# Optimization experiments

Measured on AMD Instinct MI355X. Metric: run time of the kernel, lower is better.

## Reference

```python
import jax, jax.numpy as jnp
import numpy as np

N = 768                       # atoms
E = N * (N - 1)               # complete directed graph edges
DIM = 64                      # hidden dim
CUT = 5.0                     # rbf high
NC = 50                       # n_centers = ceil(5/0.1)
ODIM = 1                      # output_dim
NCONV = 3
_centers_np = np.linspace(0.0, CUT, NC)
CENTERS = jnp.asarray(_centers_np, jnp.float32)
GAP = float(_centers_np[1] - _centers_np[0])
RO_IN = 2 * ODIM + NC         # readout input: 2*output_dim + rbf fan_out = 52


def softplus_bt(x, beta, thr):
    # torch.nn.Softplus(beta, threshold): linear above threshold
    bx = beta * x
    return jnp.where(bx > thr, x, jax.nn.softplus(bx) / beta)


def rbf(d):
    # exp(-(1/gap) * (d - mu_k)^2); d: (..., 1) -> (..., NC)
    return jnp.exp((-1.0 / GAP) * (d - CENTERS) ** 2)


def setup_inputs() -> dict:
    key = jax.random.key(0)
    ks = jax.random.split(key, 24)
    atom_types = jax.random.randint(ks[0], (N,), 0, 100)
    edge_distances = jax.random.uniform(ks[1], (E, 1), jnp.float32) * CUT
    # complete directed graph, edge order matches the nested i,j loop (i!=j)
    ii = np.repeat(np.arange(N), N)
    jj = np.tile(np.arange(N), N)
    m = ii != jj
    src = jnp.asarray(ii[m], jnp.int32)
    dst = jnp.asarray(jj[m], jnp.int32)

    def p(k, shape, fan):
        return jax.random.normal(k, shape, jnp.float32) / np.sqrt(fan)

    embedding = p(ks[2], (100, DIM), DIM).at[0].set(0.0)  # padding_idx=0
    L = NCONV
    return {
        'atom_types': atom_types, 'edge_distances': edge_distances,
        'src': src, 'dst': dst, 'embedding': embedding,
        'w1': p(ks[3], (L, DIM, DIM), DIM),                 # node_layer1 (no bias)
        'pw1': p(ks[4], (L, NC, DIM), NC), 'pb1': p(ks[5], (L, DIM), NC),
        'pw2': p(ks[6], (L, DIM, DIM), DIM), 'pb2': p(ks[7], (L, DIM), DIM),
        'qw1': p(ks[8], (L, DIM, DIM), DIM), 'qb1': p(ks[9], (L, DIM), DIM),
        'qw2': p(ks[10], (L, DIM, DIM), DIM), 'qb2': p(ks[11], (L, DIM), DIM),
        'au_w1': p(ks[12], (DIM, 64), DIM), 'au_b1': p(ks[13], (64,), DIM),
        'au_w2': p(ks[14], (64, ODIM), 64), 'au_b2': p(ks[15], (ODIM,), 64),
        'ro_w1': p(ks[16], (RO_IN, 64), RO_IN), 'ro_b1': p(ks[17], (64,), RO_IN),
        'ro_w2': p(ks[18], (64, 2), 64), 'ro_b2': p(ks[19], (2,), 64),
    }


def reference(atom_types, edge_distances, src, dst, embedding,
              w1, pw1, pb1, pw2, pb2, qw1, qb1, qw2, qb2,
              au_w1, au_b1, au_w2, au_b2, ro_w1, ro_b1, ro_w2, ro_b2):
    h = embedding[atom_types]                       # (N, DIM)
    rbf_out = rbf(edge_distances)                   # (E, NC)
    for l in range(NCONV):
        nw = h @ w1[l]                              # node weights (N, DIM)
        e = softplus_bt(rbf_out @ pw1[l] + pb1[l], 0.5, 14) @ pw2[l] + pb2[l]  # (E, DIM)
        msg = nw[src] * e                           # gather-mul (E, DIM)
        agg = jax.ops.segment_sum(msg, dst, num_segments=N)  # scatter-sum (N, DIM)
        upd = softplus_bt(agg @ qw1[l] + qb1[l], 0.5, 14) @ qw2[l] + qb2[l]
        h = h + upd
    # atom_update with ShiftSoftplus (beta=1, shift=2, threshold=20)
    ha = softplus_bt(h @ au_w1 + au_b1, 1.0, 20) - jnp.log(jnp.float32(2.0))
    ha = ha @ au_w2 + au_b2                         # (N, ODIM)
    # readout over all ordered pairs i!=j, in edge order == (src, dst)
    edge_feat = jnp.concatenate([ha[src], ha[dst], rbf_out], axis=-1)  # (E, 52)
    logits = jax.nn.relu(edge_feat @ ro_w1 + ro_b1) @ ro_w2 + ro_b2    # (E, 2)
    return jax.nn.softmax(logits, axis=-1)
```

## Files before the change

kernel.cpp:

```cpp
#include <hip/hip_runtime.h>
#include <hip/hip_fp16.h>

#define NATOMS 768
#define NM1    767
#define NEDGE  (768*767)
#define DIM    64
#define NC     50
#define GAPF   (5.0f/49.0f)
#define NIGAP  (-49.0f/5.0f)
#define G      512
#define STEPF  (5.0f/511.0f)
#define INVSTEP (511.0f/5.0f)
#define LN2F   0.693147180559945f

#define WS_H     0
#define WS_NWA   49152
#define WS_NWB   73728
#define WS_HA    98304
#define WS_DISTT 99328
#define WS_TT    689152

__device__ __forceinline__ float softplus05(float x) {
    float bx = 0.5f * x;
    return (bx > 14.0f) ? x : 2.0f * __logf(1.0f + __expf(bx));
}
__device__ __forceinline__ int lane_bcast_i(int v, int l) {
    return __builtin_amdgcn_readlane(v, l);
}
__device__ __forceinline__ float lane_bcast_f(float v, int l) {
    return __uint_as_float((unsigned)__builtin_amdgcn_readlane((int)__float_as_uint(v), l));
}

__global__ __launch_bounds__(256)
void k_pre(const int* __restrict__ types, const float* __restrict__ dist,
           const float* __restrict__ emb, const float* __restrict__ w1all,
           const float* __restrict__ pw1, const float* __restrict__ pb1,
           const float* __restrict__ pw2, const float* __restrict__ pb2,
           const float* __restrict__ row1, const float* __restrict__ rob1,
           float* __restrict__ ws) {
    __shared__ float s_t[4 * 64];
    const int tid = threadIdx.x, widx = tid >> 6, c = tid & 63;
    float*  h     = ws + WS_H;
    __half* nwh   = (__half*)(ws + WS_NWA);
    float*  distT = ws + WS_DISTT;
    __half* TTh   = (__half*)(ws + WS_TT);
    const int b = blockIdx.x;

    if (b < 512) {
        const int w = b * 4 + widx, tbl = w >> 9, g = w & 511;
        const float d = g * STEPF;
        float val;
        if (tbl < 3) {
            const float* W1 = pw1 + tbl * NC * DIM;
            float t1 = pb1[tbl * DIM + c];
            for (int k = 0; k < NC; ++k) {
                float x = d - GAPF * (float)k;
                t1 = fmaf(__expf(NIGAP * x * x), W1[k * DIM + c], t1);
            }
            s_t[widx * 64 + c] = softplus05(t1);
            const float* W2 = pw2 + tbl * DIM * DIM;
            val = pb2[tbl * DIM + c];
            #pragma unroll 8
            for (int k = 0; k < DIM; ++k)
                val = fmaf(s_t[widx * 64 + k], W2[k * DIM + c], val);
        } else {
            val = rob1[c];
            for (int k = 0; k < NC; ++k) {
                float x = d - GAPF * (float)k;
                val = fmaf(__expf(NIGAP * x * x), row1[(2 + k) * DIM + c], val);
            }
        }
        __half* TTt = TTh + tbl * (G * DIM * 2);
        TTt[(g * DIM + c) * 2] = __float2half(val);
        if (g > 0) TTt[((g - 1) * DIM + c) * 2 + 1] = __float2half(val);
    } else if (b < 704) {
        const int i = (b - 512) * 4 + widx;
        float hv = emb[types[i] * DIM + c];
        h[i * DIM + c] = hv;
        s_t[widx * 64 + c] = hv;
        float acc = 0.0f;
        #pragma unroll 8
        for (int k = 0; k < DIM; ++k)
            acc = fmaf(s_t[widx * 64 + k], w1all[k * DIM + c], acc);
        nwh[i * DIM + c] = __float2half(acc);
    } else {
        const int idx = (b - 704) * 256 + tid;
        const int j = idx / NATOMS, i = idx - j * NATOMS;
        distT[idx] = (i == j) ? 0.0f : dist[i * NM1 + (j - (j > i))];
    }
}

__global__ __launch_bounds__(512)
void k_edgeupd(const __half2* __restrict__ TTl, const float* __restrict__ distT,
               const __half* __restrict__ nwin,
               const float* __restrict__ qw1, const float* __restrict__ qb1,
               const float* __restrict__ qw2, const float* __restrict__ qb2,
               float* __restrict__ h,
               const float* __restrict__ wnext, __half* __restrict__ nwout,
               const float* __restrict__ auw1, const float* __restrict__ aub1,
               const float* __restrict__ auw2, const float* __restrict__ aub2,
               float* __restrict__ ha, int last) {
    __shared__ float s_part[8][64];
    __shared__ float s_upd[192];
    const int tid = threadIdx.x, widx = tid >> 6, c = tid & 63;
    const int j = blockIdx.x;
    const int s0 = widx * 96;

    const char* TTb = (const char*)TTl + c * 4;
    float csum = 0.0f;
    {
        float d = distT[j * NATOMS + s0 + c];
        float pos = d * INVSTEP;
        int g = (int)pos;
        g = (g < 0) ? 0 : ((g > 510) ? 510 : g);
        float f = pos - (float)g;
        int kx = g * 256;
        #pragma unroll 8
        for (int it = 0; it < 64; ++it) {
            int kxu = lane_bcast_i(kx, it);
            float fu = lane_bcast_f(f, it);
            float2 tt = __half22float2(*(const __half2*)(TTb + kxu));
            float e = fmaf(fu, tt.y - tt.x, tt.x);
            float nwv = __half2float(nwin[(s0 + it) * DIM + c]);
            csum = fmaf(e, nwv, csum);
        }
    }
    {
        float d = distT[j * NATOMS + s0 + 64 + (c & 31)];
        float pos = d * INVSTEP;
        int g = (int)pos;
        g = (g < 0) ? 0 : ((g > 510) ? 510 : g);
        float f = pos - (float)g;
        int kx = g * 256;
        #pragma unroll 8
        for (int it = 0; it < 32; ++it) {
            int kxu = lane_bcast_i(kx, it);
            float fu = lane_bcast_f(f, it);
            float2 tt = __half22float2(*(const __half2*)(TTb + kxu));
            float e = fmaf(fu, tt.y - tt.x, tt.x);
            float nwv = __half2float(nwin[(s0 + 64 + it) * DIM + c]);
            csum = fmaf(e, nwv, csum);
        }
    }
    s_part[widx][c] = csum;
    __syncthreads();

    if (widx == 0) {
        float tot = 0.0f;
        #pragma unroll
        for (int w8 = 0; w8 < 8; ++w8) tot += s_part[w8][c];
        float2 t0 = __half22float2(*(const __half2*)TTb);
        tot -= t0.x * __half2float(nwin[j * DIM + c]);
        s_upd[c] = tot;
        float t = qb1[c];
        #pragma unroll 8
        for (int k = 0; k < DIM; ++k) t = fmaf(s_upd[k], qw1[k * DIM + c], t);
        s_upd[64 + c] = softplus05(t);
        float o = qb2[c];
        #pragma unroll 8
        for (int k = 0; k < DIM; ++k) o = fmaf(s_upd[64 + k], qw2[k * DIM + c], o);
        float hn = h[j * DIM + c] + o;
        h[j * DIM + c] = hn;
        s_upd[128 + c] = hn;
        if (!last) {
            float v = 0.0f;
            #pragma unroll 8
            for (int k = 0; k < DIM; ++k) v = fmaf(s_upd[128 + k], wnext[k * DIM + c], v);
            nwout[j * DIM + c] = __float2half(v);
        } else {
            float t2 = aub1[c];
            #pragma unroll 8
            for (int k = 0; k < DIM; ++k) t2 = fmaf(s_upd[128 + k], auw1[k * DIM + c], t2);
            t2 = ((t2 > 20.0f) ? t2 : __logf(1.0f + __expf(t2))) - LN2F;
            float v = t2 * auw2[c];
            #pragma unroll
            for (int s = 32; s > 0; s >>= 1) v += __shfl_down(v, s, 64);
            if (c == 0) ha[j] = v + aub2[0];
        }
    }
}

__global__ __launch_bounds__(256)
void k_ro(const float* __restrict__ dist, const int* __restrict__ src,
          const int* __restrict__ dst, const float* __restrict__ ha,
          const __half2* __restrict__ TTro,
          const float* __restrict__ row1, const float* __restrict__ row2,
          const float* __restrict__ rob2, float* __restrict__ out) {
    __shared__ float4 s_pre[4][64];
    __shared__ float s_h[4][16 * 65];
    __shared__ float s_w2[128];
    const int tid = threadIdx.x, widx = tid >> 6, c = tid & 63;
    if (tid < 128) s_w2[tid] = row2[tid];
    __syncthreads();
    const int ebase = (blockIdx.x * 4 + widx) * 64;
    {
        int eg = ebase + c;
        float d = dist[eg];
        float pos = d * INVSTEP;
        int kk = (int)pos;
        kk = (kk < 0) ? 0 : ((kk > 510) ? 510 : kk);
        float fa = ha[src[eg]], fb = ha[dst[eg]];
        s_pre[widx][c] = make_float4(__int_as_float(kk * 256), pos - (float)kk, fa, fb);
    }
    const char* TTb2 = (const char*)TTro + c * 4;
    const float wa = row1[c], wb = row1[DIM + c];
    const int e2 = (c >> 1) & 15, p2 = c & 1, kh = c >> 5;
    const float bias2 = (kh == 0) ? rob2[p2] : 0.0f;
    float* sh = s_h[widx];
    #pragma unroll
    for (int ch = 0; ch < 4; ++ch) {
        #pragma unroll 4
        for (int e = 0; e < 16; ++e) {
            float4 p = s_pre[widx][ch * 16 + e];
            float2 tt = __half22float2(*(const __half2*)(TTb2 + __float_as_int(p.x)));
            float hv = fmaf(p.y, tt.y - tt.x, tt.x);
            hv = fmaf(p.z, wa, hv);
            hv = fmaf(p.w, wb, hv);
            sh[e * 65 + c] = fmaxf(hv, 0.0f);
        }
        float lsum = bias2;
        #pragma unroll 8
        for (int k8 = 0; k8 < 32; ++k8) {
            int k = kh * 32 + k8;
            lsum = fmaf(sh[e2 * 65 + k], s_w2[2 * k + p2], lsum);
        }
        lsum += __shfl_xor(lsum, 32, 64);
        float other = __shfl_xor(lsum, 1, 64);
        float m = fmaxf(lsum, other);
        float ea = __expf(lsum - m), eb = __expf(other - m);
        float r = ea / (ea + eb);
        if (c < 32) out[ebase * 2 + ch * 32 + c] = r;
    }
}

extern "C" void kernel_launch(void* const* d_in, const int* in_sizes, int n_in,
                              void* d_out, int out_size, void* d_ws, size_t ws_size,
                              hipStream_t stream) {
    const int*   types = (const int*)d_in[0];
    const float* dist  = (const float*)d_in[1];
    const int*   srcI  = (const int*)d_in[2];
    const int*   dstI  = (const int*)d_in[3];
    const float* emb   = (const float*)d_in[4];
    const float* w1    = (const float*)d_in[5];
    const float* pw1   = (const float*)d_in[6];
    const float* pb1   = (const float*)d_in[7];
    const float* pw2   = (const float*)d_in[8];
    const float* pb2   = (const float*)d_in[9];
    const float* qw1   = (const float*)d_in[10];
    const float* qb1   = (const float*)d_in[11];
    const float* qw2   = (const float*)d_in[12];
    const float* qb2   = (const float*)d_in[13];
    const float* auw1  = (const float*)d_in[14];
    const float* aub1  = (const float*)d_in[15];
    const float* auw2  = (const float*)d_in[16];
    const float* aub2  = (const float*)d_in[17];
    const float* row1  = (const float*)d_in[18];
    const float* rob1  = (const float*)d_in[19];
    const float* row2  = (const float*)d_in[20];
    const float* rob2  = (const float*)d_in[21];

    float* ws   = (float*)d_ws;
    float* outp = (float*)d_out;
    const __half2* TT = (const __half2*)(ws + WS_TT);
    __half* nwbuf[2] = { (__half*)(ws + WS_NWA), (__half*)(ws + WS_NWB) };

    k_pre<<<3008, 256, 0, stream>>>(types, dist, emb, w1, pw1, pb1, pw2, pb2,
                                    row1, rob1, ws);
    for (int l = 0; l < 3; ++l) {
        k_edgeupd<<<768, 512, 0, stream>>>(TT + l * (G * DIM),
            ws + WS_DISTT, nwbuf[l & 1],
            qw1 + l * DIM * DIM, qb1 + l * DIM,
            qw2 + l * DIM * DIM, qb2 + l * DIM,
            ws + WS_H,
            (l < 2) ? (w1 + (l + 1) * DIM * DIM) : w1, nwbuf[(l + 1) & 1],
            auw1, aub1, auw2, aub2, ws + WS_HA, (l == 2) ? 1 : 0);
    }
    k_ro<<<2301, 256, 0, stream>>>(dist, srcI, dstI, ws + WS_HA, TT + 3 * (G * DIM),
                                   row1, row2, rob2, outp);
}
```

Measured before the change: 189.5 us.

## Stage edge-filter lookup table in LDS and process three atoms per block

The per-layer half-precision interpolation table (512x64 pairs, 128 KB) is now copied into shared memory once per block, and lookups read LDS instead of global/L2. Each block handles three destination atoms to spread the copy cost, so the grid shrinks from 768 to 256 blocks, and three waves then run the per-atom MLP update in parallel. The trade-off is 128 KB+ of LDS per block, which limits occupancy to one block per CU, and only 256 blocks on a large GPU with a serial load phase before any compute.

New measurement: 207.8 us. 1.1x slower.

```diff
diff --git a/kernel.cpp b/kernel.cpp
--- a/kernel.cpp
+++ b/kernel.cpp
@@ -29,6 +29,10 @@
 }
 __device__ __forceinline__ float lane_bcast_f(float v, int l) {
     return __uint_as_float((unsigned)__builtin_amdgcn_readlane((int)__float_as_uint(v), l));
+}
+__device__ __forceinline__ float2 pair2f(unsigned p) {
+    __half2 h = *reinterpret_cast<__half2*>(&p);
+    return __half22float2(h);
 }
 
 __global__ __launch_bounds__(256)
@@ -91,7 +95,7 @@
 }
 
 __global__ __launch_bounds__(512)
-void k_edgeupd(const __half2* __restrict__ TTl, const float* __restrict__ distT,
+void k_edgeupd(const unsigned* __restrict__ TTl, const float* __restrict__ distT,
                const __half* __restrict__ nwin,
                const float* __restrict__ qw1, const float* __restrict__ qb1,
                const float* __restrict__ qw2, const float* __restrict__ qb2,
@@ -100,77 +104,93 @@
                const float* __restrict__ auw1, const float* __restrict__ aub1,
                const float* __restrict__ auw2, const float* __restrict__ aub2,
                float* __restrict__ ha, int last) {
-    __shared__ float s_part[8][64];
-    __shared__ float s_upd[192];
+    __shared__ unsigned s_tab[G * DIM];
+    __shared__ float s_part[3][8][64];
+    __shared__ float s_upd[3][192];
     const int tid = threadIdx.x, widx = tid >> 6, c = tid & 63;
-    const int j = blockIdx.x;
+    const int b = blockIdx.x;
     const int s0 = widx * 96;
 
-    const char* TTb = (const char*)TTl + c * 4;
-    float csum = 0.0f;
     {
-        float d = distT[j * NATOMS + s0 + c];
-        float pos = d * INVSTEP;
-        int g = (int)pos;
-        g = (g < 0) ? 0 : ((g > 510) ? 510 : g);
-        float f = pos - (float)g;
-        int kx = g * 256;
-        #pragma unroll 8
-        for (int it = 0; it < 64; ++it) {
-            int kxu = lane_bcast_i(kx, it);
-            float fu = lane_bcast_f(f, it);
-            float2 tt = __half22float2(*(const __half2*)(TTb + kxu));
-            float e = fmaf(fu, tt.y - tt.x, tt.x);
-            float nwv = __half2float(nwin[(s0 + it) * DIM + c]);
-            csum = fmaf(e, nwv, csum);
-        }
-    }
-    {
-        float d = distT[j * NATOMS + s0 + 64 + (c & 31)];
-        float pos = d * INVSTEP;
-        int g = (int)pos;
-        g = (g < 0) ? 0 : ((g > 510) ? 510 : g);
-        float f = pos - (float)g;
-        int kx = g * 256;
-        #pragma unroll 8
-        for (int it = 0; it < 32; ++it) {
-            int kxu = lane_bcast_i(kx, it);
-            float fu = lane_bcast_f(f, it);
-            float2 tt = __half22float2(*(const __half2*)(TTb + kxu));
-            float e = fmaf(fu, tt.y - tt.x, tt.x);
-            float nwv = __half2float(nwin[(s0 + 64 + it) * DIM + c]);
-            csum = fmaf(e, nwv, csum);
-        }
-    }
-    s_part[widx][c] = csum;
+        const uint4* src = (const uint4*)TTl;
+        uint4* dst = (uint4*)s_tab;
+        #pragma unroll
+        for (int it = 0; it < 16; ++it)
+            dst[tid + it * 512] = src[tid + it * 512];
+    }
     __syncthreads();
 
-    if (widx == 0) {
+    for (int dd = 0; dd < 3; ++dd) {
+        const int j = b * 3 + dd;
+        const float* drow = distT + j * NATOMS;
+        float csum = 0.0f;
+        {
+            float d = drow[s0 + c];
+            float pos = d * INVSTEP;
+            int g = (int)pos;
+            g = (g < 0) ? 0 : ((g > 510) ? 510 : g);
+            float f = pos - (float)g;
+            int kw = g << 6;
+            #pragma unroll 8
+            for (int it = 0; it < 64; ++it) {
+                int kwu = lane_bcast_i(kw, it);
+                float fu = lane_bcast_f(f, it);
+                float2 tt = pair2f(s_tab[kwu + c]);
+                float e = fmaf(fu, tt.y - tt.x, tt.x);
+                float nwv = __half2float(nwin[(s0 + it) * DIM + c]);
+                csum = fmaf(e, nwv, csum);
+            }
+        }
+        {
+            float d = drow[s0 + 64 + (c & 31)];
+            float pos = d * INVSTEP;
+            int g = (int)pos;
+            g = (g < 0) ? 0 : ((g > 510) ? 510 : g);
+            float f = pos - (float)g;
+            int kw = g << 6;
+            #pragma unroll 8
+            for (int it = 0; it < 32; ++it) {
+                int kwu = lane_bcast_i(kw, it);
+                float fu = lane_bcast_f(f, it);
+                float2 tt = pair2f(s_tab[kwu + c]);
+                float e = fmaf(fu, tt.y - tt.x, tt.x);
+                float nwv = __half2float(nwin[(s0 + 64 + it) * DIM + c]);
+                csum = fmaf(e, nwv, csum);
+            }
+        }
+        s_part[dd][widx][c] = csum;
+    }
+    __syncthreads();
+
+    if (widx < 3) {
+        const int dd = widx;
+        const int j = b * 3 + dd;
         float tot = 0.0f;
         #pragma unroll
-        for (int w8 = 0; w8 < 8; ++w8) tot += s_part[w8][c];
-        float2 t0 = __half22float2(*(const __half2*)TTb);
+        for (int w8 = 0; w8 < 8; ++w8) tot += s_part[dd][w8][c];
+        float2 t0 = pair2f(s_tab[c]);
         tot -= t0.x * __half2float(nwin[j * DIM + c]);
-        s_upd[c] = tot;
+        float* su = s_upd[dd];
+        su[c] = tot;
         float t = qb1[c];
         #pragma unroll 8
-        for (int k = 0; k < DIM; ++k) t = fmaf(s_upd[k], qw1[k * DIM + c], t);
-        s_upd[64 + c] = softplus05(t);
+        for (int k = 0; k < DIM; ++k) t = fmaf(su[k], qw1[k * DIM + c], t);
+        su[64 + c] = softplus05(t);
         float o = qb2[c];
         #pragma unroll 8
-        for (int k = 0; k < DIM; ++k) o = fmaf(s_upd[64 + k], qw2[k * DIM + c], o);
+        for (int k = 0; k < DIM; ++k) o = fmaf(su[64 + k], qw2[k * DIM + c], o);
         float hn = h[j * DIM + c] + o;
         h[j * DIM + c] = hn;
-        s_upd[128 + c] = hn;
+        su[128 + c] = hn;
         if (!last) {
             float v = 0.0f;
             #pragma unroll 8
-            for (int k = 0; k < DIM; ++k) v = fmaf(s_upd[128 + k], wnext[k * DIM + c], v);
+            for (int k = 0; k < DIM; ++k) v = fmaf(su[128 + k], wnext[k * DIM + c], v);
             nwout[j * DIM + c] = __float2half(v);
         } else {
             float t2 = aub1[c];
             #pragma unroll 8
-            for (int k = 0; k < DIM; ++k) t2 = fmaf(s_upd[128 + k], auw1[k * DIM + c], t2);
+            for (int k = 0; k < DIM; ++k) t2 = fmaf(su[128 + k], auw1[k * DIM + c], t2);
             t2 = ((t2 > 20.0f) ? t2 : __logf(1.0f + __expf(t2))) - LN2F;
             float v = t2 * auw2[c];
             #pragma unroll
@@ -261,13 +281,13 @@
 
     float* ws   = (float*)d_ws;
     float* outp = (float*)d_out;
-    const __half2* TT = (const __half2*)(ws + WS_TT);
+    const unsigned* TT = (const unsigned*)(ws + WS_TT);
     __half* nwbuf[2] = { (__half*)(ws + WS_NWA), (__half*)(ws + WS_NWB) };
 
     k_pre<<<3008, 256, 0, stream>>>(types, dist, emb, w1, pw1, pb1, pw2, pb2,
                                     row1, rob1, ws);
     for (int l = 0; l < 3; ++l) {
-        k_edgeupd<<<768, 512, 0, stream>>>(TT + l * (G * DIM),
+        k_edgeupd<<<256, 512, 0, stream>>>(TT + l * (G * DIM),
             ws + WS_DISTT, nwbuf[l & 1],
             qw1 + l * DIM * DIM, qb1 + l * DIM,
             qw2 + l * DIM * DIM, qb2 + l * DIM,
@@ -275,6 +295,7 @@
             (l < 2) ? (w1 + (l + 1) * DIM * DIM) : w1, nwbuf[(l + 1) & 1],
             auw1, aub1, auw2, aub2, ws + WS_HA, (l == 2) ? 1 : 0);
     }
-    k_ro<<<2301, 256, 0, stream>>>(dist, srcI, dstI, ws + WS_HA, TT + 3 * (G * DIM),
+    k_ro<<<2301, 256, 0, stream>>>(dist, srcI, dstI, ws + WS_HA,
+                                   (const __half2*)(TT + 3 * (G * DIM)),
                                    row1, row2, rob2, outp);
 }
```
